# Kernel tuning notes

Hardware: AMD Instinct MI355X
Metric: run time of the kernel (lower is better)

## Reference

```python
import jax, jax.numpy as jnp
import numpy as np


def setup_inputs() -> dict:
    key = jax.random.key(0)
    kx, kw = jax.random.split(key)
    B, IN, OUT = 8192, 1024, 4096
    x = jax.random.normal(kx, (B, IN), dtype=jnp.float32)
    # torch.rand -> uniform [0,1)
    weight = jax.random.uniform(kw, (IN, OUT), dtype=jnp.float32)
    return {"x": x, "weight": weight}


def reference(x, weight):
    # Faithful to: (x.unsqueeze(-1) - weight).pow(2).sum(-2)
    # i.e. out[b, o] = sum_i (x[b, i] - weight[i, o])**2
    # Computed via the squared-distance expansion to avoid the
    # (B, in, out) broadcast intermediate:
    x_sq = jnp.sum(x * x, axis=-1, keepdims=True)          # (B, 1)
    w_sq = jnp.sum(weight * weight, axis=0)                # (OUT,)
    cross = jnp.matmul(x, weight)                          # (B, OUT)
    return x_sq - 2.0 * cross + w_sq
```

## Files before the change

kernel.cpp:

```cpp
#include <hip/hip_runtime.h>
#include <cstdint>
#include <cstddef>

#define B_DIM   8192
#define IN_DIM  1024
#define OUT_DIM 4096
#define KT2     (IN_DIM / 64)

typedef __attribute__((ext_vector_type(8)))  int   i32x8;
typedef __attribute__((ext_vector_type(4)))  int   i32x4;
typedef __attribute__((ext_vector_type(16))) float f32x16;

__device__ __forceinline__ void async_copy16(const void* gptr, void* ldsptr) {
    __builtin_amdgcn_global_load_lds(
        (__attribute__((address_space(1))) void*)gptr,
        (__attribute__((address_space(3))) void*)ldsptr,
        16, 0, 0);
}

__device__ __forceinline__ int pack4_fp8(float a, float b, float c, float d) {
    int pk = __builtin_amdgcn_cvt_pk_fp8_f32(a, b, 0, false);
    pk = __builtin_amdgcn_cvt_pk_fp8_f32(c, d, pk, true);
    return pk;
}


__global__ __launch_bounds__(256) void tile_x_kernel(
    const float* __restrict__ x, unsigned char* __restrict__ At,
    float* __restrict__ xsq, float* __restrict__ wsq)
{
    const int t = threadIdx.x;
    const int w = t >> 6;
    const int l = t & 63;
    const int mt = blockIdx.x;
    const int m  = mt * 32 + (l & 31);

    float s = 0.0f;
    #pragma unroll
    for (int c = 0; c < 4; ++c) {
        const int kt2 = c * 4 + w;
        const float* src = x + (size_t)m * IN_DIM + kt2 * 64 + (l >> 5) * 32;
        i32x4 lo, hi;
        #pragma unroll
        for (int j = 0; j < 4; ++j) {
            float4 v = ((const float4*)src)[j];
            s += v.x*v.x + v.y*v.y + v.z*v.z + v.w*v.w;
            lo[j] = pack4_fp8(v.x, v.y, v.z, v.w);
        }
        #pragma unroll
        for (int j = 0; j < 4; ++j) {
            float4 v = ((const float4*)src)[4 + j];
            s += v.x*v.x + v.y*v.y + v.z*v.z + v.w*v.w;
            hi[j] = pack4_fp8(v.x, v.y, v.z, v.w);
        }
        unsigned char* pan = At + ((size_t)mt * KT2 + kt2) * 2048;
        *(i32x4*)(pan + l * 16)        = lo;
        *(i32x4*)(pan + 1024 + l * 16) = hi;
    }
    s += __shfl_down(s, 32, 64);
    __shared__ float red[4][32];
    if (l < 32) red[w][l] = s;
    __syncthreads();
    if (t < 32) xsq[mt * 32 + t] = red[0][t] + red[1][t] + red[2][t] + red[3][t];

    if (blockIdx.x < OUT_DIM / 256) wsq[blockIdx.x * 256 + t] = 0.0f;
}

__global__ __launch_bounds__(256) void tile_w_kernel(
    const float* __restrict__ wgt, unsigned char* __restrict__ Bt,
    float* __restrict__ wsq)
{
    __shared__ float tile[256 * 33];
    const int t  = threadIdx.x;
    const int w  = t >> 6;
    const int l  = t & 63;
    const int nt = blockIdx.x;
    const int q  = blockIdx.y;
    const int n0 = nt * 32;

    {
        const int rbase = t >> 2, cg = (t & 3) * 8;
        #pragma unroll
        for (int rep = 0; rep < 4; ++rep) {
            const int r = rbase + rep * 64;
            const float* src = wgt + (size_t)(q * 256 + r) * OUT_DIM + n0 + cg;
            float4 v0 = ((const float4*)src)[0];
            float4 v1 = ((const float4*)src)[1];
            float* d = &tile[r * 33 + cg];
            d[0] = v0.x; d[1] = v0.y; d[2] = v0.z; d[3] = v0.w;
            d[4] = v1.x; d[5] = v1.y; d[6] = v1.z; d[7] = v1.w;
        }
    }
    __syncthreads();

    const int kt2 = q * 4 + w;
    const int n   = l & 31;
    const int kb  = w * 64 + (l >> 5) * 32;
    float s = 0.0f;
    i32x4 lo, hi;
    #pragma unroll
    for (int j4 = 0; j4 < 4; ++j4) {
        float f0 = tile[(kb + j4 * 4 + 0) * 33 + n];
        float f1 = tile[(kb + j4 * 4 + 1) * 33 + n];
        float f2 = tile[(kb + j4 * 4 + 2) * 33 + n];
        float f3 = tile[(kb + j4 * 4 + 3) * 33 + n];
        s += f0*f0 + f1*f1 + f2*f2 + f3*f3;
        lo[j4] = pack4_fp8(f0, f1, f2, f3);
    }
    #pragma unroll
    for (int j4 = 0; j4 < 4; ++j4) {
        float f0 = tile[(kb + 16 + j4 * 4 + 0) * 33 + n];
        float f1 = tile[(kb + 16 + j4 * 4 + 1) * 33 + n];
        float f2 = tile[(kb + 16 + j4 * 4 + 2) * 33 + n];
        float f3 = tile[(kb + 16 + j4 * 4 + 3) * 33 + n];
        s += f0*f0 + f1*f1 + f2*f2 + f3*f3;
        hi[j4] = pack4_fp8(f0, f1, f2, f3);
    }
    unsigned char* pan = Bt + ((size_t)nt * KT2 + kt2) * 2048;
    *(i32x4*)(pan + l * 16)        = lo;
    *(i32x4*)(pan + 1024 + l * 16) = hi;

    s += __shfl_down(s, 32, 64);
    __shared__ float red[4][32];
    if (l < 32) red[w][l] = s;
    __syncthreads();
    if (t < 32) atomicAdd(&wsq[n0 + t], red[0][t] + red[1][t] + red[2][t] + red[3][t]);
}

__global__ __launch_bounds__(256) void rbf_gemm_kernel(
    const unsigned char* __restrict__ At,
    const unsigned char* __restrict__ Bt,
    const float* __restrict__ xsq,
    const float* __restrict__ wsq,
    float* __restrict__ out)
{
    __shared__ __align__(16) unsigned char sm[2][32768];

    const int t    = threadIdx.x;
    const int w    = t >> 6;
    const int l    = t & 63;
    const int l32  = l & 31;
    const int half = l >> 5;
    const int bm = blockIdx.x;
    const int bn = blockIdx.y;
    const int waveRow = w >> 1;
    const int waveCol = w & 1;

    f32x16 acc[2][2];
    #pragma unroll
    for (int mi = 0; mi < 2; ++mi)
        #pragma unroll
        for (int ni = 0; ni < 2; ++ni)
            #pragma unroll
            for (int r = 0; r < 16; ++r)
                acc[mi][ni][r] = 0.0f;

    auto stage = [&](int buf, int kti) {
        unsigned char* As = sm[buf];
        unsigned char* Bs = sm[buf] + 16384;
        #pragma unroll
        for (int pp = 0; pp < 2; ++pp) {
            const int p = w * 2 + pp;
            const unsigned char* ga = At + ((size_t)(bm * 4 + w) * KT2 + kti * 2 + pp) * 2048;
            const unsigned char* gb = Bt + ((size_t)(bn * 4 + w) * KT2 + kti * 2 + pp) * 2048;
            #pragma unroll
            for (int h = 0; h < 2; ++h) {
                async_copy16(ga + h * 1024 + l * 16, As + p * 2048 + h * 1024);
                async_copy16(gb + h * 1024 + l * 16, Bs + p * 2048 + h * 1024);
            }
        }
    };

    auto ldfrag = [&](const unsigned char* base, int p) -> i32x8 {
        i32x4 lo = *(const i32x4*)(base + p * 2048 + l * 16);
        i32x4 hi = *(const i32x4*)(base + p * 2048 + 1024 + l * 16);
        i32x8 r;
        r[0] = lo[0]; r[1] = lo[1]; r[2] = lo[2]; r[3] = lo[3];
        r[4] = hi[0]; r[5] = hi[1]; r[6] = hi[2]; r[7] = hi[3];
        return r;
    };

    stage(0, 0);
    __syncthreads();

    for (int kti = 0; kti < 8; ++kti) {
        if (kti < 7) stage((kti + 1) & 1, kti + 1);

        const unsigned char* As = sm[kti & 1];
        const unsigned char* Bs = sm[kti & 1] + 16384;
        #pragma unroll
        for (int ks = 0; ks < 2; ++ks) {
            i32x8 af[2], bf[2];
            #pragma unroll
            for (int mi = 0; mi < 2; ++mi)
                af[mi] = ldfrag(As, (waveRow * 2 + mi) * 2 + ks);
            #pragma unroll
            for (int ni = 0; ni < 2; ++ni)
                bf[ni] = ldfrag(Bs, (waveCol * 2 + ni) * 2 + ks);
            #pragma unroll
            for (int mi = 0; mi < 2; ++mi)
                #pragma unroll
                for (int ni = 0; ni < 2; ++ni)
                    acc[mi][ni] = __builtin_amdgcn_mfma_scale_f32_32x32x64_f8f6f4(
                        af[mi], bf[ni], acc[mi][ni],
                        0, 0,
                        0, 0x7F7F7F7F,
                        0, 0x7F7F7F7F);
        }
        __syncthreads();
    }

    #pragma unroll
    for (int mi = 0; mi < 2; ++mi) {
        const int mbase = bm * 128 + waveRow * 64 + mi * 32 + 4 * half;
        #pragma unroll
        for (int r2 = 0; r2 < 4; ++r2) {
            #pragma unroll
            for (int r1 = 0; r1 < 4; ++r1) {
                const int m  = mbase + r1 + 8 * r2;
                const float xs = xsq[m];
                #pragma unroll
                for (int ni = 0; ni < 2; ++ni) {
                    const int n = bn * 128 + waveCol * 64 + ni * 32 + l32;
                    out[(size_t)m * OUT_DIM + n] =
                        xs + wsq[n] - 2.0f * acc[mi][ni][r2 * 4 + r1];
                }
            }
        }
    }
}

extern "C" void kernel_launch(void* const* d_in, const int* in_sizes, int n_in,
                              void* d_out, int out_size, void* d_ws, size_t ws_size,
                              hipStream_t stream)
{
    const float* x   = (const float*)d_in[0];
    const float* wgt = (const float*)d_in[1];
    float* out = (float*)d_out;
    char*  ws  = (char*)d_ws;

    unsigned char* At = (unsigned char*)ws;
    unsigned char* Bt = (unsigned char*)(ws + (size_t)B_DIM * IN_DIM);
    float* xsq = (float*)(ws + (size_t)B_DIM * IN_DIM + (size_t)OUT_DIM * IN_DIM);
    float* wsq = xsq + B_DIM;

    tile_x_kernel<<<B_DIM / 32, 256, 0, stream>>>(x, At, xsq, wsq);
    tile_w_kernel<<<dim3(OUT_DIM / 32, 4), 256, 0, stream>>>(wgt, Bt, wsq);
    rbf_gemm_kernel<<<dim3(B_DIM / 128, OUT_DIM / 128), 256, 0, stream>>>(At, Bt, xsq, wsq, out);
}
```

Before: 201.7 us.

## Load B fragments directly from global into registers with prefetch, bypassing LDS

The B operand is no longer staged through shared memory. Each wave loads its B MFMA fragments straight from the pre-tiled global buffer into registers, one k-tile ahead, while A keeps the double-buffered LDS async path. This halves LDS traffic and footprint, which may raise occupancy. In exchange, B loads are duplicated across the two waves that share a column, which adds global/L2 traffic and register pressure.

New measurement: 202.8 us. No clear change (+0.6%).

```diff
diff --git a/kernel.cpp b/kernel.cpp
--- a/kernel.cpp
+++ b/kernel.cpp
@@ -134,7 +134,7 @@
     const float* __restrict__ wsq,
     float* __restrict__ out)
 {
-    __shared__ __align__(16) unsigned char sm[2][32768];
+    __shared__ __align__(16) unsigned char smA[2][16384];
 
     const int t    = threadIdx.x;
     const int w    = t >> 6;
@@ -155,23 +155,30 @@
             for (int r = 0; r < 16; ++r)
                 acc[mi][ni][r] = 0.0f;
 
-    auto stage = [&](int buf, int kti) {
-        unsigned char* As = sm[buf];
-        unsigned char* Bs = sm[buf] + 16384;
+    auto stageA = [&](int buf, int kti) {
         #pragma unroll
         for (int pp = 0; pp < 2; ++pp) {
-            const int p = w * 2 + pp;
-            const unsigned char* ga = At + ((size_t)(bm * 4 + w) * KT2 + kti * 2 + pp) * 2048;
-            const unsigned char* gb = Bt + ((size_t)(bn * 4 + w) * KT2 + kti * 2 + pp) * 2048;
-            #pragma unroll
-            for (int h = 0; h < 2; ++h) {
-                async_copy16(ga + h * 1024 + l * 16, As + p * 2048 + h * 1024);
-                async_copy16(gb + h * 1024 + l * 16, Bs + p * 2048 + h * 1024);
-            }
+            const unsigned char* ga =
+                At + ((size_t)(bm * 4 + w) * KT2 + kti * 2 + pp) * 2048;
+            unsigned char* ld = smA[buf] + (w * 2 + pp) * 2048;
+            async_copy16(ga + l * 16,        ld);
+            async_copy16(ga + 1024 + l * 16, ld + 1024);
         }
     };
 
-    auto ldfrag = [&](const unsigned char* base, int p) -> i32x8 {
+    auto ldB = [&](int ni, int kti, int ks) -> i32x8 {
+        const unsigned char* gb =
+            Bt + ((size_t)(bn * 4 + waveCol * 2 + ni) * KT2 + kti * 2 + ks) * 2048
+               + l * 16;
+        i32x4 lo = *(const i32x4*)gb;
+        i32x4 hi = *(const i32x4*)(gb + 1024);
+        i32x8 r;
+        r[0] = lo[0]; r[1] = lo[1]; r[2] = lo[2]; r[3] = lo[3];
+        r[4] = hi[0]; r[5] = hi[1]; r[6] = hi[2]; r[7] = hi[3];
+        return r;
+    };
+
+    auto ldA = [&](const unsigned char* base, int p) -> i32x8 {
         i32x4 lo = *(const i32x4*)(base + p * 2048 + l * 16);
         i32x4 hi = *(const i32x4*)(base + p * 2048 + 1024 + l * 16);
         i32x8 r;
@@ -180,34 +187,48 @@
         return r;
     };
 
-    stage(0, 0);
+    stageA(0, 0);
+    i32x8 bcur[2][2];
+    #pragma unroll
+    for (int ks = 0; ks < 2; ++ks)
+        #pragma unroll
+        for (int ni = 0; ni < 2; ++ni)
+            bcur[ks][ni] = ldB(ni, 0, ks);
     __syncthreads();
 
     for (int kti = 0; kti < 8; ++kti) {
-        if (kti < 7) stage((kti + 1) & 1, kti + 1);
-
-        const unsigned char* As = sm[kti & 1];
-        const unsigned char* Bs = sm[kti & 1] + 16384;
+        if (kti < 7) stageA((kti + 1) & 1, kti + 1);
+        const int nk = (kti < 7) ? kti + 1 : 7;
+        i32x8 bnxt[2][2];
+        #pragma unroll
+        for (int ks = 0; ks < 2; ++ks)
+            #pragma unroll
+            for (int ni = 0; ni < 2; ++ni)
+                bnxt[ks][ni] = ldB(ni, nk, ks);
+
+        const unsigned char* As = smA[kti & 1];
         #pragma unroll
         for (int ks = 0; ks < 2; ++ks) {
-            i32x8 af[2], bf[2];
+            i32x8 af[2];
             #pragma unroll
             for (int mi = 0; mi < 2; ++mi)
-                af[mi] = ldfrag(As, (waveRow * 2 + mi) * 2 + ks);
-            #pragma unroll
-            for (int ni = 0; ni < 2; ++ni)
-                bf[ni] = ldfrag(Bs, (waveCol * 2 + ni) * 2 + ks);
+                af[mi] = ldA(As, (waveRow * 2 + mi) * 2 + ks);
             #pragma unroll
             for (int mi = 0; mi < 2; ++mi)
                 #pragma unroll
                 for (int ni = 0; ni < 2; ++ni)
                     acc[mi][ni] = __builtin_amdgcn_mfma_scale_f32_32x32x64_f8f6f4(
-                        af[mi], bf[ni], acc[mi][ni],
+                        af[mi], bcur[ks][ni], acc[mi][ni],
                         0, 0,
                         0, 0x7F7F7F7F,
                         0, 0x7F7F7F7F);
         }
         __syncthreads();
+        #pragma unroll
+        for (int ks = 0; ks < 2; ++ks)
+            #pragma unroll
+            for (int ni = 0; ni < 2; ++ni)
+                bcur[ks][ni] = bnxt[ks][ni];
     }
 
     #pragma unroll
```
